# Performance work log

Measured on AMD Instinct MI355X. Metric: run time of the kernel, lower is better.

Reference implementation:

```python
import jax, jax.numpy as jnp
import numpy as np

N = 50000      # nodes
E = 800000     # edges (before self loops)
IN = 128       # in_dim
HID = 128      # hidden
H = 4          # heads
C = HID // H   # per-head channels = 32
G = 512        # graphs in batch
NEG_SLOPE = 0.2


def setup_inputs() -> dict:
    key = jax.random.key(0)
    ks = jax.random.split(key, 20)
    inp = {}
    inp["x"] = jax.random.normal(ks[0], (N, IN), jnp.float32)
    inp["edge_index"] = jax.random.randint(ks[1], (2, E), 0, N, dtype=jnp.int32)
    inp["edge_attr"] = jax.random.normal(ks[2], (E, 8), jnp.float32)
    inp["batch"] = jnp.sort(jax.random.randint(ks[3], (N,), 0, G, dtype=jnp.int32))
    dims = [IN, HID, HID]
    for i in range(3):
        s = 1.0 / np.sqrt(dims[i])
        inp[f"conv{i}_W"] = jax.random.normal(ks[4 + 4 * i], (dims[i], HID), jnp.float32) * s
        inp[f"conv{i}_att_src"] = jax.random.normal(ks[5 + 4 * i], (H, C), jnp.float32) * 0.1
        inp[f"conv{i}_att_dst"] = jax.random.normal(ks[6 + 4 * i], (H, C), jnp.float32) * 0.1
        inp[f"conv{i}_b"] = jnp.zeros((HID,), jnp.float32)
    inp["mlp_W1"] = jax.random.normal(ks[16], (HID, HID), jnp.float32) / np.sqrt(HID)
    inp["mlp_b1"] = jnp.zeros((HID,), jnp.float32)
    inp["mlp_W2"] = jax.random.normal(ks[17], (HID, 1), jnp.float32) / np.sqrt(HID)
    inp["mlp_b2"] = jnp.zeros((1,), jnp.float32)
    return inp


def _gat_conv(x, W, att_src, att_dst, b, src, dst, n):
    # linear transform -> per-head features [n, H, C]
    h = (x @ W).reshape(n, H, C)
    a_src = jnp.einsum("nhc,hc->nh", h, att_src)  # [n, H]
    a_dst = jnp.einsum("nhc,hc->nh", h, att_dst)
    e = jax.nn.leaky_relu(a_src[src] + a_dst[dst], NEG_SLOPE)  # [Etot, H]
    # segment softmax over edges sharing the same destination node
    m = jax.ops.segment_max(e, dst, num_segments=n)
    ex = jnp.exp(e - m[dst])
    denom = jax.ops.segment_sum(ex, dst, num_segments=n)
    alpha = ex / denom[dst]                                     # [Etot, H]
    msg = h[src] * alpha[..., None]                             # [Etot, H, C]
    out = jax.ops.segment_sum(msg, dst, num_segments=n)        # [n, H, C]
    return out.reshape(n, HID) + b


def reference(x, edge_index, edge_attr, batch,
              conv0_W, conv0_att_src, conv0_att_dst, conv0_b,
              conv1_W, conv1_att_src, conv1_att_dst, conv1_b,
              conv2_W, conv2_att_src, conv2_att_dst, conv2_b,
              mlp_W1, mlp_b1, mlp_W2, mlp_b2):
    n = x.shape[0]
    loops = jnp.arange(n, dtype=edge_index.dtype)  # PyG GATConv adds self-loops
    src = jnp.concatenate([edge_index[0], loops])
    dst = jnp.concatenate([edge_index[1], loops])
    convs = [
        (conv0_W, conv0_att_src, conv0_att_dst, conv0_b),
        (conv1_W, conv1_att_src, conv1_att_dst, conv1_b),
        (conv2_W, conv2_att_src, conv2_att_dst, conv2_b),
    ]
    h = x
    for (W, a_s, a_d, b) in convs:
        h = jax.nn.elu(_gat_conv(h, W, a_s, a_d, b, src, dst, n))
        # dropout is identity in eval mode
    # global mean pool over graphs
    sums = jax.ops.segment_sum(h, batch, num_segments=G)                  # [G, HID]
    cnts = jax.ops.segment_sum(jnp.ones((n,), h.dtype), batch, num_segments=G)
    g = sums / jnp.maximum(cnts, 1.0)[:, None]
    g = jax.nn.relu(g @ mlp_W1 + mlp_b1)
    return g @ mlp_W2 + mlp_b2  # [G, 1]
```

## Files before the change

### kernel.cpp

```cpp
#include <hip/hip_runtime.h>
#include <math.h>

#define N_NODES 50000
#define E_EDGES 800000
#define ETOT    (E_EDGES + N_NODES)
#define HIDF    128
#define HEADS   4
#define CH      32
#define G_GRAPHS 512
#define NEG_SLOPE 0.2f
#define KSLC 32

#define SC_ELEMS  1024
#define SC_BLOCKS ((N_NODES + SC_ELEMS - 1) / SC_ELEMS)

__global__ __launch_bounds__(256) void gemm_att(const float* __restrict__ A,
                                                const float* __restrict__ W,
                                                const float* __restrict__ att_src,
                                                const float* __restrict__ att_dst,
                                                float* __restrict__ out,
                                                float* __restrict__ a_src,
                                                float* __restrict__ a_dst, int n) {
    __shared__ float Ws[KSLC][128];
    __shared__ float As[64][132];
    const int t = threadIdx.x;
    const int row0 = blockIdx.x * 64;

#pragma unroll
    for (int i = 0; i < 8; i++) {
        int idx = t + 256 * i;
        int r = idx >> 5, c4 = idx & 31;
        float4 v = make_float4(0.f, 0.f, 0.f, 0.f);
        if (row0 + r < n) v = ((const float4*)A)[(size_t)(row0 + r) * 32 + c4];
        *(float4*)&As[r][c4 * 4] = v;
    }

    const int tr = t >> 4;
    const int tc = t & 15;
    float acc[4][8];
#pragma unroll
    for (int i = 0; i < 4; i++)
#pragma unroll
        for (int j = 0; j < 8; j++) acc[i][j] = 0.f;

    const float4* W4 = (const float4*)W;
    for (int ks = 0; ks < 128; ks += KSLC) {
        __syncthreads();
#pragma unroll
        for (int i = 0; i < 4; i++) {
            int idx = t + 256 * i;
            int kk = idx >> 5, c4 = idx & 31;
            *(float4*)&Ws[kk][c4 * 4] = W4[(size_t)(ks + kk) * 32 + c4];
        }
        __syncthreads();

#pragma unroll
        for (int k = 0; k < KSLC; k += 4) {
            float a[4][4];
#pragma unroll
            for (int i = 0; i < 4; i++)
                *(float4*)&a[i][0] = *(const float4*)&As[tr * 4 + i][ks + k];
#pragma unroll
            for (int kk = 0; kk < 4; kk++) {
                float4 w0 = *(const float4*)&Ws[k + kk][tc * 8];
                float4 w1 = *(const float4*)&Ws[k + kk][tc * 8 + 4];
#pragma unroll
                for (int i = 0; i < 4; i++) {
                    float av = a[i][kk];
                    acc[i][0] += av * w0.x; acc[i][1] += av * w0.y;
                    acc[i][2] += av * w0.z; acc[i][3] += av * w0.w;
                    acc[i][4] += av * w1.x; acc[i][5] += av * w1.y;
                    acc[i][6] += av * w1.z; acc[i][7] += av * w1.w;
                }
            }
        }
    }

#pragma unroll
    for (int i = 0; i < 4; i++) {
        int r = row0 + tr * 4 + i;
        if (r < n) {
            float* op = out + (size_t)r * 128 + tc * 8;
            *(float4*)op       = make_float4(acc[i][0], acc[i][1], acc[i][2], acc[i][3]);
            *(float4*)(op + 4) = make_float4(acc[i][4], acc[i][5], acc[i][6], acc[i][7]);
        }
    }

    const int hd = tc >> 2;
    const int jo = hd * CH + (tc & 3) * 8;
    float sv[8], dv[8];
    *(float4*)&sv[0] = *(const float4*)&att_src[jo];
    *(float4*)&sv[4] = *(const float4*)&att_src[jo + 4];
    *(float4*)&dv[0] = *(const float4*)&att_dst[jo];
    *(float4*)&dv[4] = *(const float4*)&att_dst[jo + 4];

    __syncthreads();
    float* red2 = &As[0][0];
#pragma unroll
    for (int i = 0; i < 4; i++) {
        float ps = 0.f, pd = 0.f;
#pragma unroll
        for (int j = 0; j < 8; j++) { ps += acc[i][j] * sv[j]; pd += acc[i][j] * dv[j]; }
        red2[(tr * 4 + i) * 32 + tc * 2]     = ps;
        red2[(tr * 4 + i) * 32 + tc * 2 + 1] = pd;
    }
    __syncthreads();

    {
        int r = t >> 2, hd2 = t & 3;
        float ps = 0.f, pd = 0.f;
#pragma unroll
        for (int q = 0; q < 4; q++) {
            ps += red2[r * 32 + (hd2 * 4 + q) * 2];
            pd += red2[r * 32 + (hd2 * 4 + q) * 2 + 1];
        }
        int row = row0 + r;
        if (row < n) {
            a_src[row * 4 + hd2] = ps;
            a_dst[row * 4 + hd2] = pd;
        }
    }
}

__global__ void hist_k(const int* __restrict__ ei, int* __restrict__ cnt) {
    int e = blockIdx.x * blockDim.x + threadIdx.x;
    if (e >= ETOT) return;
    int d = (e < E_EDGES) ? ei[E_EDGES + e] : e - E_EDGES;
    atomicAdd(&cnt[d], 1);
}

__global__ __launch_bounds__(256) void scan_bsum(const int* __restrict__ cnt,
                                                 int* __restrict__ bsum) {
    int b = blockIdx.x, t = threadIdx.x;
    int base = b * SC_ELEMS + t * 4;
    int s = 0;
#pragma unroll
    for (int q = 0; q < 4; q++) { int idx = base + q; if (idx < N_NODES) s += cnt[idx]; }
    __shared__ int red[256];
    red[t] = s;
    __syncthreads();
    for (int st = 128; st > 0; st >>= 1) {
        if (t < st) red[t] += red[t + st];
        __syncthreads();
    }
    if (t == 0) bsum[b] = red[0];
}

__global__ __launch_bounds__(64) void scan_boff(const int* __restrict__ bsum,
                                                int* __restrict__ boff,
                                                int* __restrict__ rowptr_last) {
    int t = threadIdx.x;
    int v = (t < SC_BLOCKS) ? bsum[t] : 0;
    int incl = v;
#pragma unroll
    for (int off = 1; off < 64; off <<= 1) {
        int u = __shfl_up(incl, off);
        if (t >= off) incl += u;
    }
    if (t < SC_BLOCKS) boff[t] = incl - v;
    if (t == 63) rowptr_last[0] = incl;
}

__global__ __launch_bounds__(256) void scan_write(const int* __restrict__ cnt,
                                                  const int* __restrict__ boff,
                                                  int* __restrict__ rowptr) {
    int b = blockIdx.x, t = threadIdx.x;
    int base = b * SC_ELEMS + t * 4;
    int v[4]; int s = 0;
#pragma unroll
    for (int q = 0; q < 4; q++) { int idx = base + q; v[q] = (idx < N_NODES) ? cnt[idx] : 0; s += v[q]; }
    __shared__ int red[256];
    red[t] = s;
    __syncthreads();
    for (int off = 1; off < 256; off <<= 1) {
        int u = (t >= off) ? red[t - off] : 0;
        __syncthreads();
        red[t] += u;
        __syncthreads();
    }
    int run = boff[b] + red[t] - s;
#pragma unroll
    for (int q = 0; q < 4; q++) {
        int idx = base + q;
        if (idx < N_NODES) rowptr[idx] = run;
        run += v[q];
    }
}

__global__ void fill_k(const int* __restrict__ ei, const int* __restrict__ rowptr,
                       int* __restrict__ cursor, int* __restrict__ col) {
    int e = blockIdx.x * blockDim.x + threadIdx.x;
    if (e >= ETOT) return;
    int s, d;
    if (e < E_EDGES) { s = ei[e]; d = ei[E_EDGES + e]; }
    else             { s = d = e - E_EDGES; }
    int pos = atomicAdd(&cursor[d], 1);
    col[rowptr[d] + pos] = s;
}

__global__ __launch_bounds__(256) void gat_wave(const float* __restrict__ h,
                                                const float4* __restrict__ a_src4,
                                                const float4* __restrict__ a_dst4,
                                                const int* __restrict__ rowptr,
                                                const int* __restrict__ col,
                                                const float* __restrict__ bias,
                                                float* __restrict__ out) {
    const int wid  = (blockIdx.x * 256 + threadIdx.x) >> 6;
    const int lane = threadIdx.x & 63;
    if (wid >= N_NODES) return;
    const int beg = rowptr[wid], end = rowptr[wid + 1];
    const float4 ad = a_dst4[wid];
    const int part = lane & 15;
    const int egrp = lane >> 4;
    const int head = part >> 2;

    float acc[8];
#pragma unroll
    for (int j = 0; j < 8; j++) acc[j] = 0.f;
    float4 den = make_float4(0.f, 0.f, 0.f, 0.f);

    for (int base = beg; base < end; base += 64) {
        int i = base + lane;
        int s = 0;
        float4 ex = make_float4(0.f, 0.f, 0.f, 0.f);
        if (i < end) {
            s = col[i];
            float4 as = a_src4[s];
            float vx = as.x + ad.x, vy = as.y + ad.y, vz = as.z + ad.z, vw = as.w + ad.w;
            vx = vx > 0.f ? vx : NEG_SLOPE * vx;
            vy = vy > 0.f ? vy : NEG_SLOPE * vy;
            vz = vz > 0.f ? vz : NEG_SLOPE * vz;
            vw = vw > 0.f ? vw : NEG_SLOPE * vw;
            ex = make_float4(__expf(vx), __expf(vy), __expf(vz), __expf(vw));
            den.x += ex.x; den.y += ex.y; den.z += ex.z; den.w += ex.w;
        }
        int cnt = end - base; if (cnt > 64) cnt = 64;
        int quads = (cnt + 3) >> 2;
        for (int k = 0; k < quads; k++) {
            int src_lane = 4 * k + egrp;
            int   sk = __shfl(s, src_lane);
            float e0 = __shfl(ex.x, src_lane);
            float e1 = __shfl(ex.y, src_lane);
            float e2 = __shfl(ex.z, src_lane);
            float e3 = __shfl(ex.w, src_lane);
            float aV = head == 0 ? e0 : head == 1 ? e1 : head == 2 ? e2 : e3;
            const float4* hp = (const float4*)(h + (size_t)sk * HIDF + part * 8);
            float4 v0 = hp[0], v1 = hp[1];
            acc[0] += aV * v0.x; acc[1] += aV * v0.y;
            acc[2] += aV * v0.z; acc[3] += aV * v0.w;
            acc[4] += aV * v1.x; acc[5] += aV * v1.y;
            acc[6] += aV * v1.z; acc[7] += aV * v1.w;
        }
    }

#pragma unroll
    for (int j = 0; j < 8; j++) {
        acc[j] += __shfl_xor(acc[j], 16);
        acc[j] += __shfl_xor(acc[j], 32);
    }
#pragma unroll
    for (int off = 32; off > 0; off >>= 1) {
        den.x += __shfl_xor(den.x, off);
        den.y += __shfl_xor(den.y, off);
        den.z += __shfl_xor(den.z, off);
        den.w += __shfl_xor(den.w, off);
    }
    float d = head == 0 ? den.x : head == 1 ? den.y : head == 2 ? den.z : den.w;
    float inv = 1.f / d;

    if (lane < 16) {
        const float* bp = bias + part * 8;
        float o[8];
#pragma unroll
        for (int j = 0; j < 8; j++) {
            float v = acc[j] * inv + bp[j];
            o[j] = v > 0.f ? v : expm1f(v);
        }
        float* op = out + (size_t)wid * HIDF + part * 8;
        *(float4*)op       = make_float4(o[0], o[1], o[2], o[3]);
        *(float4*)(op + 4) = make_float4(o[4], o[5], o[6], o[7]);
    }
}

__global__ void gstart_k(const int* __restrict__ batch, int* __restrict__ gstart) {
    int i = blockIdx.x * blockDim.x + threadIdx.x;
    if (i >= N_NODES) return;
    int b = batch[i];
    int bp = (i == 0) ? -1 : batch[i - 1];
    for (int g = bp + 1; g <= b; g++) gstart[g] = i;
    if (i == N_NODES - 1)
        for (int g = b + 1; g <= G_GRAPHS; g++) gstart[g] = N_NODES;
}

__global__ __launch_bounds__(128) void pool_mlp(const float* __restrict__ h,
                                                const int* __restrict__ gstart,
                                                const float* __restrict__ W1,
                                                const float* __restrict__ b1,
                                                const float* __restrict__ W2,
                                                const float* __restrict__ b2,
                                                float* __restrict__ out) {
    int g = blockIdx.x, j = threadIdx.x;
    int s = gstart[g], e = gstart[g + 1];
    float acc = 0.f;
    for (int i = s; i < e; i++) acc += h[(size_t)i * HIDF + j];
    float c = (float)(e - s); c = c > 1.f ? c : 1.f;
    __shared__ float gv[128];
    __shared__ float red[128];
    gv[j] = acc / c;
    __syncthreads();
    float a1 = b1[j];
    for (int k = 0; k < 128; k++) a1 += gv[k] * W1[k * 128 + j];
    a1 = a1 > 0.f ? a1 : 0.f;
    red[j] = a1 * W2[j];
    __syncthreads();
    for (int st = 64; st > 0; st >>= 1) {
        if (j < st) red[j] += red[j + st];
        __syncthreads();
    }
    if (j == 0) out[g] = red[0] + b2[0];
}

extern "C" void kernel_launch(void* const* d_in, const int* in_sizes, int n_in,
                              void* d_out, int out_size, void* d_ws, size_t ws_size,
                              hipStream_t stream) {
    const float* x   = (const float*)d_in[0];
    const int* ei    = (const int*)d_in[1];
    const int* batch = (const int*)d_in[3];
    const float* convW[3]  = { (const float*)d_in[4],  (const float*)d_in[8],  (const float*)d_in[12] };
    const float* convAS[3] = { (const float*)d_in[5],  (const float*)d_in[9],  (const float*)d_in[13] };
    const float* convAD[3] = { (const float*)d_in[6],  (const float*)d_in[10], (const float*)d_in[14] };
    const float* convB[3]  = { (const float*)d_in[7],  (const float*)d_in[11], (const float*)d_in[15] };
    const float* mlp_W1 = (const float*)d_in[16];
    const float* mlp_b1 = (const float*)d_in[17];
    const float* mlp_W2 = (const float*)d_in[18];
    const float* mlp_b2 = (const float*)d_in[19];
    float* out = (float*)d_out;

    float* ws = (float*)d_ws;
    float* bufA  = ws;
    float* bufB  = bufA + (size_t)N_NODES * HIDF;
    float* a_src = bufB + (size_t)N_NODES * HIDF;
    float* a_dst = a_src + (size_t)N_NODES * HEADS;
    int* cnt     = (int*)(a_dst + (size_t)N_NODES * HEADS);
    int* rowptr  = cnt + N_NODES;
    int* col     = rowptr + (N_NODES + 1);
    int* gstart  = col + ETOT;
    int* bsum    = gstart + (G_GRAPHS + 1);
    int* boff    = bsum + SC_BLOCKS;

    const int B = 256;
    const int gridGemm = (N_NODES + 63) / 64;
    const int gridEtot = (ETOT + B - 1) / B;
    const int gridWave = (N_NODES * 64 + B - 1) / B;
    const int gridN    = (N_NODES + B - 1) / B;

    hipMemsetAsync(cnt, 0, (size_t)N_NODES * sizeof(int), stream);
    hist_k<<<gridEtot, B, 0, stream>>>(ei, cnt);
    scan_bsum<<<SC_BLOCKS, 256, 0, stream>>>(cnt, bsum);
    scan_boff<<<1, 64, 0, stream>>>(bsum, boff, rowptr + N_NODES);
    scan_write<<<SC_BLOCKS, 256, 0, stream>>>(cnt, boff, rowptr);
    hipMemsetAsync(cnt, 0, (size_t)N_NODES * sizeof(int), stream);
    fill_k<<<gridEtot, B, 0, stream>>>(ei, rowptr, cnt, col);
    gstart_k<<<gridN, B, 0, stream>>>(batch, gstart);

    const float* cur = x;
    for (int L = 0; L < 3; L++) {
        gemm_att<<<gridGemm, B, 0, stream>>>(cur, convW[L], convAS[L], convAD[L],
                                             bufA, a_src, a_dst, N_NODES);
        gat_wave<<<gridWave, B, 0, stream>>>(bufA, (const float4*)a_src, (const float4*)a_dst,
                                             rowptr, col, convB[L], bufB);
        cur = bufB;
    }

    pool_mlp<<<G_GRAPHS, 128, 0, stream>>>(bufB, gstart, mlp_W1, mlp_b1, mlp_W2, mlp_b2, out);
}
```

Before: 571.2 us.

## Enlarge GEMM tile to 128 rows with 8x8 register blocking and transposed A staging

The fused GEMM-plus-attention kernel now processes 128 rows per block instead of 64. Each thread accumulates an 8x8 outer product in registers. A is staged per K-slice, transposed into shared memory with a padded stride, so both operands come from shared memory as vector reads. This raises arithmetic intensity and halves the grid, at the cost of more registers per thread. The padded stride of 133 makes the float4 shared-memory accesses misaligned, which is a correctness and performance risk.

```diff
diff --git a/kernel.cpp b/kernel.cpp
--- a/kernel.cpp
+++ b/kernel.cpp
@@ -21,29 +21,23 @@
                                                 float* __restrict__ out,
                                                 float* __restrict__ a_src,
                                                 float* __restrict__ a_dst, int n) {
-    __shared__ float Ws[KSLC][128];
-    __shared__ float As[64][132];
+    __shared__ float As[KSLC][133];
+    __shared__ float Ws[KSLC][133];
     const int t = threadIdx.x;
-    const int row0 = blockIdx.x * 64;
-
-#pragma unroll
-    for (int i = 0; i < 8; i++) {
-        int idx = t + 256 * i;
-        int r = idx >> 5, c4 = idx & 31;
-        float4 v = make_float4(0.f, 0.f, 0.f, 0.f);
-        if (row0 + r < n) v = ((const float4*)A)[(size_t)(row0 + r) * 32 + c4];
-        *(float4*)&As[r][c4 * 4] = v;
-    }
+    const int row0 = blockIdx.x * 128;
 
     const int tr = t >> 4;
     const int tc = t & 15;
-    float acc[4][8];
-#pragma unroll
-    for (int i = 0; i < 4; i++)
+
+    float acc[8][8];
+#pragma unroll
+    for (int i = 0; i < 8; i++)
 #pragma unroll
         for (int j = 0; j < 8; j++) acc[i][j] = 0.f;
 
     const float4* W4 = (const float4*)W;
+    const float4* A4 = (const float4*)A;
+
     for (int ks = 0; ks < 128; ks += KSLC) {
         __syncthreads();
 #pragma unroll
@@ -52,33 +46,37 @@
             int kk = idx >> 5, c4 = idx & 31;
             *(float4*)&Ws[kk][c4 * 4] = W4[(size_t)(ks + kk) * 32 + c4];
         }
-        __syncthreads();
-
-#pragma unroll
-        for (int k = 0; k < KSLC; k += 4) {
-            float a[4][4];
-#pragma unroll
-            for (int i = 0; i < 4; i++)
-                *(float4*)&a[i][0] = *(const float4*)&As[tr * 4 + i][ks + k];
-#pragma unroll
-            for (int kk = 0; kk < 4; kk++) {
-                float4 w0 = *(const float4*)&Ws[k + kk][tc * 8];
-                float4 w1 = *(const float4*)&Ws[k + kk][tc * 8 + 4];
-#pragma unroll
-                for (int i = 0; i < 4; i++) {
-                    float av = a[i][kk];
-                    acc[i][0] += av * w0.x; acc[i][1] += av * w0.y;
-                    acc[i][2] += av * w0.z; acc[i][3] += av * w0.w;
-                    acc[i][4] += av * w1.x; acc[i][5] += av * w1.y;
-                    acc[i][6] += av * w1.z; acc[i][7] += av * w1.w;
-                }
-            }
-        }
-    }
-
-#pragma unroll
-    for (int i = 0; i < 4; i++) {
-        int r = row0 + tr * 4 + i;
+#pragma unroll
+        for (int i = 0; i < 4; i++) {
+            int r  = (t >> 3) + 32 * i;
+            int kq = t & 7;
+            float4 v = make_float4(0.f, 0.f, 0.f, 0.f);
+            if (row0 + r < n) v = A4[(size_t)(row0 + r) * 32 + (ks >> 2) + kq];
+            As[kq * 4 + 0][r] = v.x;
+            As[kq * 4 + 1][r] = v.y;
+            As[kq * 4 + 2][r] = v.z;
+            As[kq * 4 + 3][r] = v.w;
+        }
+        __syncthreads();
+
+#pragma unroll
+        for (int kk = 0; kk < KSLC; kk++) {
+            float4 a0 = *(const float4*)&As[kk][tr * 8];
+            float4 a1 = *(const float4*)&As[kk][tr * 8 + 4];
+            float4 w0 = *(const float4*)&Ws[kk][tc * 8];
+            float4 w1 = *(const float4*)&Ws[kk][tc * 8 + 4];
+            float av[8] = {a0.x, a0.y, a0.z, a0.w, a1.x, a1.y, a1.z, a1.w};
+            float wv[8] = {w0.x, w0.y, w0.z, w0.w, w1.x, w1.y, w1.z, w1.w};
+#pragma unroll
+            for (int i = 0; i < 8; i++)
+#pragma unroll
+                for (int j = 0; j < 8; j++) acc[i][j] += av[i] * wv[j];
+        }
+    }
+
+#pragma unroll
+    for (int i = 0; i < 8; i++) {
+        int r = row0 + tr * 8 + i;
         if (r < n) {
             float* op = out + (size_t)r * 128 + tc * 8;
             *(float4*)op       = make_float4(acc[i][0], acc[i][1], acc[i][2], acc[i][3]);
@@ -97,17 +95,19 @@
     __syncthreads();
     float* red2 = &As[0][0];
 #pragma unroll
-    for (int i = 0; i < 4; i++) {
+    for (int i = 0; i < 8; i++) {
         float ps = 0.f, pd = 0.f;
 #pragma unroll
         for (int j = 0; j < 8; j++) { ps += acc[i][j] * sv[j]; pd += acc[i][j] * dv[j]; }
-        red2[(tr * 4 + i) * 32 + tc * 2]     = ps;
-        red2[(tr * 4 + i) * 32 + tc * 2 + 1] = pd;
-    }
-    __syncthreads();
-
-    {
-        int r = t >> 2, hd2 = t & 3;
+        red2[(tr * 8 + i) * 32 + tc * 2]     = ps;
+        red2[(tr * 8 + i) * 32 + tc * 2 + 1] = pd;
+    }
+    __syncthreads();
+
+#pragma unroll
+    for (int rr = 0; rr < 2; rr++) {
+        int idx = t + 256 * rr;
+        int r = idx >> 2, hd2 = idx & 3;
         float ps = 0.f, pd = 0.f;
 #pragma unroll
         for (int q = 0; q < 4; q++) {
@@ -349,7 +349,7 @@
     int* boff    = bsum + SC_BLOCKS;
 
     const int B = 256;
-    const int gridGemm = (N_NODES + 63) / 64;
+    const int gridGemm = (N_NODES + 127) / 128;
     const int gridEtot = (ETOT + B - 1) / B;
     const int gridWave = (N_NODES * 64 + B - 1) / B;
     const int gridN    = (N_NODES + B - 1) / B;
```

Measured after the change: 640.9 us. 1.12x slower.

## Split GAT aggregation across two waves per node and fold counter reset into scan

Applied to the files above, without the earlier changes.

The aggregation kernel now gives each destination node two wavefronts, one per pair of heads (64 channels each). Each lane loads one float4 of source features per edge instead of two, and holds 4 accumulators instead of 8. This doubles the wave count, which should expose more parallelism and memory-level concurrency, but the col indices, a_src values and exp computations are now loaded and evaluated twice per edge. Separately, scan_write zeroes the count array after reading it, which removes one memset launch before fill_k.

```diff
diff --git a/kernel.cpp b/kernel.cpp
--- a/kernel.cpp
+++ b/kernel.cpp
@@ -161,14 +161,18 @@
     if (t == 63) rowptr_last[0] = incl;
 }
 
-__global__ __launch_bounds__(256) void scan_write(const int* __restrict__ cnt,
+__global__ __launch_bounds__(256) void scan_write(int* __restrict__ cnt,
                                                   const int* __restrict__ boff,
                                                   int* __restrict__ rowptr) {
     int b = blockIdx.x, t = threadIdx.x;
     int base = b * SC_ELEMS + t * 4;
     int v[4]; int s = 0;
 #pragma unroll
-    for (int q = 0; q < 4; q++) { int idx = base + q; v[q] = (idx < N_NODES) ? cnt[idx] : 0; s += v[q]; }
+    for (int q = 0; q < 4; q++) {
+        int idx = base + q;
+        v[q] = (idx < N_NODES) ? cnt[idx] : 0; s += v[q];
+        if (idx < N_NODES) cnt[idx] = 0;
+    }
     __shared__ int red[256];
     red[t] = s;
     __syncthreads();
@@ -199,40 +203,40 @@
 }
 
 __global__ __launch_bounds__(256) void gat_wave(const float* __restrict__ h,
-                                                const float4* __restrict__ a_src4,
-                                                const float4* __restrict__ a_dst4,
+                                                const float2* __restrict__ a_src2,
+                                                const float2* __restrict__ a_dst2,
                                                 const int* __restrict__ rowptr,
                                                 const int* __restrict__ col,
                                                 const float* __restrict__ bias,
                                                 float* __restrict__ out) {
-    const int wid  = (blockIdx.x * 256 + threadIdx.x) >> 6;
+    const int gw   = (blockIdx.x * 256 + threadIdx.x) >> 6;
     const int lane = threadIdx.x & 63;
+    const int wid  = gw >> 1;
+    const int half = gw & 1;
     if (wid >= N_NODES) return;
     const int beg = rowptr[wid], end = rowptr[wid + 1];
-    const float4 ad = a_dst4[wid];
+    const float2 ad = a_dst2[wid * 2 + half];
     const int part = lane & 15;
     const int egrp = lane >> 4;
-    const int head = part >> 2;
-
-    float acc[8];
-#pragma unroll
-    for (int j = 0; j < 8; j++) acc[j] = 0.f;
-    float4 den = make_float4(0.f, 0.f, 0.f, 0.f);
+    const int hsel = part >> 3;
+
+    float acc[4];
+#pragma unroll
+    for (int j = 0; j < 4; j++) acc[j] = 0.f;
+    float2 den = make_float2(0.f, 0.f);
 
     for (int base = beg; base < end; base += 64) {
         int i = base + lane;
         int s = 0;
-        float4 ex = make_float4(0.f, 0.f, 0.f, 0.f);
+        float2 ex = make_float2(0.f, 0.f);
         if (i < end) {
             s = col[i];
-            float4 as = a_src4[s];
-            float vx = as.x + ad.x, vy = as.y + ad.y, vz = as.z + ad.z, vw = as.w + ad.w;
+            float2 as = a_src2[s * 2 + half];
+            float vx = as.x + ad.x, vy = as.y + ad.y;
             vx = vx > 0.f ? vx : NEG_SLOPE * vx;
             vy = vy > 0.f ? vy : NEG_SLOPE * vy;
-            vz = vz > 0.f ? vz : NEG_SLOPE * vz;
-            vw = vw > 0.f ? vw : NEG_SLOPE * vw;
-            ex = make_float4(__expf(vx), __expf(vy), __expf(vz), __expf(vw));
-            den.x += ex.x; den.y += ex.y; den.z += ex.z; den.w += ex.w;
+            ex = make_float2(__expf(vx), __expf(vy));
+            den.x += ex.x; den.y += ex.y;
         }
         int cnt = end - base; if (cnt > 64) cnt = 64;
         int quads = (cnt + 3) >> 2;
@@ -241,20 +245,15 @@
             int   sk = __shfl(s, src_lane);
             float e0 = __shfl(ex.x, src_lane);
             float e1 = __shfl(ex.y, src_lane);
-            float e2 = __shfl(ex.z, src_lane);
-            float e3 = __shfl(ex.w, src_lane);
-            float aV = head == 0 ? e0 : head == 1 ? e1 : head == 2 ? e2 : e3;
-            const float4* hp = (const float4*)(h + (size_t)sk * HIDF + part * 8);
-            float4 v0 = hp[0], v1 = hp[1];
-            acc[0] += aV * v0.x; acc[1] += aV * v0.y;
-            acc[2] += aV * v0.z; acc[3] += aV * v0.w;
-            acc[4] += aV * v1.x; acc[5] += aV * v1.y;
-            acc[6] += aV * v1.z; acc[7] += aV * v1.w;
-        }
-    }
-
-#pragma unroll
-    for (int j = 0; j < 8; j++) {
+            float aV = hsel == 0 ? e0 : e1;
+            float4 v = *(const float4*)(h + (size_t)sk * HIDF + half * 64 + part * 4);
+            acc[0] += aV * v.x; acc[1] += aV * v.y;
+            acc[2] += aV * v.z; acc[3] += aV * v.w;
+        }
+    }
+
+#pragma unroll
+    for (int j = 0; j < 4; j++) {
         acc[j] += __shfl_xor(acc[j], 16);
         acc[j] += __shfl_xor(acc[j], 32);
     }
@@ -262,23 +261,20 @@
     for (int off = 32; off > 0; off >>= 1) {
         den.x += __shfl_xor(den.x, off);
         den.y += __shfl_xor(den.y, off);
-        den.z += __shfl_xor(den.z, off);
-        den.w += __shfl_xor(den.w, off);
-    }
-    float d = head == 0 ? den.x : head == 1 ? den.y : head == 2 ? den.z : den.w;
+    }
+    float d = hsel == 0 ? den.x : den.y;
     float inv = 1.f / d;
 
     if (lane < 16) {
-        const float* bp = bias + part * 8;
-        float o[8];
-#pragma unroll
-        for (int j = 0; j < 8; j++) {
+        const float* bp = bias + half * 64 + part * 4;
+        float o[4];
+#pragma unroll
+        for (int j = 0; j < 4; j++) {
             float v = acc[j] * inv + bp[j];
             o[j] = v > 0.f ? v : expm1f(v);
         }
-        float* op = out + (size_t)wid * HIDF + part * 8;
-        *(float4*)op       = make_float4(o[0], o[1], o[2], o[3]);
-        *(float4*)(op + 4) = make_float4(o[4], o[5], o[6], o[7]);
+        *(float4*)(out + (size_t)wid * HIDF + half * 64 + part * 4) =
+            make_float4(o[0], o[1], o[2], o[3]);
     }
 }
 
@@ -351,7 +347,7 @@
     const int B = 256;
     const int gridGemm = (N_NODES + 63) / 64;
     const int gridEtot = (ETOT + B - 1) / B;
-    const int gridWave = (N_NODES * 64 + B - 1) / B;
+    const int gridWave = (N_NODES * 2 * 64 + B - 1) / B;
     const int gridN    = (N_NODES + B - 1) / B;
 
     hipMemsetAsync(cnt, 0, (size_t)N_NODES * sizeof(int), stream);
@@ -359,7 +355,6 @@
     scan_bsum<<<SC_BLOCKS, 256, 0, stream>>>(cnt, bsum);
     scan_boff<<<1, 64, 0, stream>>>(bsum, boff, rowptr + N_NODES);
     scan_write<<<SC_BLOCKS, 256, 0, stream>>>(cnt, boff, rowptr);
-    hipMemsetAsync(cnt, 0, (size_t)N_NODES * sizeof(int), stream);
     fill_k<<<gridEtot, B, 0, stream>>>(ei, rowptr, cnt, col);
     gstart_k<<<gridN, B, 0, stream>>>(batch, gstart);
 
@@ -367,7 +362,7 @@
     for (int L = 0; L < 3; L++) {
         gemm_att<<<gridGemm, B, 0, stream>>>(cur, convW[L], convAS[L], convAD[L],
                                              bufA, a_src, a_dst, N_NODES);
-        gat_wave<<<gridWave, B, 0, stream>>>(bufA, (const float4*)a_src, (const float4*)a_dst,
+        gat_wave<<<gridWave, B, 0, stream>>>(bufA, (const float2*)a_src, (const float2*)a_dst,
                                              rowptr, col, convB[L], bufB);
         cur = bufB;
     }
```

Result: no change. 579.5 us (+1.5%).
